# Optimization experiments

Hardware: AMD Instinct MI355X
Metric: run time of the kernel (lower is better)

Reference implementation:

```python
import jax, jax.numpy as jnp
import numpy as np

N, D, C = 8192, 256, 100
MARGIN = 1.0


def setup_inputs() -> dict:
    key = jax.random.key(0)
    k1, k2 = jax.random.split(key)
    features = jax.random.normal(k1, (N, D), dtype=jnp.float32)
    labels = jax.random.randint(k2, (N,), 0, C, dtype=jnp.int64)
    return {"features": features, "labels": labels}


def _pairwise_dist(f):
    # f: [N, D] L2-normalized rows. Euclidean distance matrix [N, N].
    sq = jnp.sum(f * f, axis=1)  # [N]
    d2 = sq[:, None] + sq[None, :] - 2.0 * (f @ f.T)
    d2 = jnp.maximum(d2, 0.0)
    # safe sqrt: zero distance (incl. diagonal) -> 0 with finite grad
    pos = d2 > 0.0
    return jnp.where(pos, jnp.sqrt(jnp.where(pos, d2, 1.0)), 0.0)


def reference(features, labels):
    # F.normalize(p=2, dim=1)
    norm = jnp.linalg.norm(features, axis=1, keepdims=True)
    f = features / jnp.maximum(norm, 1e-12)

    dist = _pairwise_dist(f)  # [N, N]

    onehot = jax.nn.one_hot(labels, C, dtype=f.dtype)  # [N, C]
    counts = jnp.sum(onehot, axis=0)  # [C]
    # S[a, b] = sum_{i in a, j in b} dist[i, j]
    S = onehot.T @ dist @ onehot  # [C, C]

    # intra: per-class mean over off-diagonal pairs (diag of dist is 0),
    # only classes with count > 1, then mean over those classes
    intra_valid = counts > 1.0
    intra_denom = jnp.where(intra_valid, counts * (counts - 1.0), 1.0)
    intra_per_class = jnp.diag(S) / intra_denom
    n_intra = jnp.sum(intra_valid.astype(f.dtype))
    intra = jnp.where(
        n_intra > 0,
        jnp.sum(jnp.where(intra_valid, intra_per_class, 0.0)) / jnp.maximum(n_intra, 1.0),
        0.0,
    )

    # inter: per class-pair (a < b, both present) mean distance, then mean over pairs
    pair_cnt = counts[:, None] * counts[None, :]
    inter_mat = S / jnp.where(pair_cnt > 0.0, pair_cnt, 1.0)
    present = counts > 0.0
    upper = jnp.triu(jnp.ones((C, C), dtype=bool), k=1)
    pair_mask = upper & present[:, None] & present[None, :]
    n_pairs = jnp.sum(pair_mask.astype(f.dtype))
    inter = jnp.where(
        n_pairs > 0,
        jnp.sum(jnp.where(pair_mask, inter_mat, 0.0)) / jnp.maximum(n_pairs, 1.0),
        1.0,
    )

    loss = jax.nn.relu(intra - inter + MARGIN)
    return loss  # scalar; .mean() of a scalar is itself
```

## Files before the change

### kernel.cpp

```cpp
#include <hip/hip_runtime.h>
#include <math.h>

#define N_ROWS 8192
#define D_DIM  256
#define C_CLS  100
#define BM 128
#define BK 128
#define NSTRIP (N_ROWS / BM)
#define NBLK (NSTRIP * (NSTRIP + 1) / 2)
#define UPK (C_CLS * (C_CLS + 1) / 2)
#define MAXSEG 4

typedef __attribute__((ext_vector_type(4))) float floatx4;

__device__ __forceinline__ void gl2lds16(const void* g, void* l) {
    __builtin_amdgcn_global_load_lds(
        (const __attribute__((address_space(1))) void*)g,
        (__attribute__((address_space(3))) void*)l, 16, 0, 0);
}

__global__ void sort_k(const int* __restrict__ labels, int* __restrict__ dest,
                       int* __restrict__ slab, int* __restrict__ offs,
                       float* __restrict__ Ug) {
    __shared__ int h[C_CLS];
    __shared__ int oS[C_CLS + 1];
    __shared__ int cur[C_CLS];
    const int t = threadIdx.x;
    if (t < C_CLS) h[t] = 0;
    __syncthreads();
    int myl[8];
#pragma unroll
    for (int u = 0; u < 8; ++u) myl[u] = labels[t + u * 1024];
#pragma unroll
    for (int u = 0; u < 8; ++u) atomicAdd(&h[myl[u]], 1);
    __syncthreads();
    if (t == 0) {
        int run = 0;
        for (int c = 0; c < C_CLS; ++c) { oS[c] = run; run += h[c]; }
        oS[C_CLS] = run;
    }
    __syncthreads();
    if (t < C_CLS) cur[t] = oS[t];
    __syncthreads();
#pragma unroll
    for (int u = 0; u < 8; ++u) {
        const int i = t + u * 1024;
        const int pos = atomicAdd(&cur[myl[u]], 1);
        dest[i] = pos;
        slab[pos] = myl[u];
    }
    if (t < C_CLS + 1) offs[t] = oS[t];
    for (int e = t; e < UPK; e += 1024) Ug[e] = 0.f;
}

__global__ void normalize_k(const float* __restrict__ in, const int* __restrict__ dest,
                            unsigned int* __restrict__ fnb8) {
    const int row  = blockIdx.x * 4 + (threadIdx.x >> 6);
    const int lane = threadIdx.x & 63;
    float4 v = ((const float4*)in)[row * 64 + lane];
    float s = v.x * v.x + v.y * v.y + v.z * v.z + v.w * v.w;
#pragma unroll
    for (int o = 32; o > 0; o >>= 1) s += __shfl_xor(s, o, 64);
    const float inv = 1.f / fmaxf(sqrtf(s), 1e-12f);
    const int d = dest[row];
    int pk = __builtin_amdgcn_cvt_pk_fp8_f32(v.x * inv, v.y * inv, 0, 0);
    pk     = __builtin_amdgcn_cvt_pk_fp8_f32(v.z * inv, v.w * inv, pk, 1);
    fnb8[d * 64 + lane] = (unsigned int)pk;
}

__global__ __launch_bounds__(256, 4)
void main_k(const unsigned char* __restrict__ fnb8, const int* __restrict__ slab,
            const int* __restrict__ offs_g, float* __restrict__ Ug) {
    __shared__ __align__(16) unsigned char As[BM * BK];
    __shared__ __align__(16) unsigned char Bs[BM * BK];
    __shared__ float red[4][MAXSEG * MAXSEG][17];
    __shared__ int soffs[C_CLS + 1];
    __shared__ int meta[4][4];

    const int t = threadIdx.x;

    int b = blockIdx.x, ti = 0, len = NSTRIP;
    while (b >= len) { b -= len; ++ti; --len; }
    const int tj = ti + b;
    const int i0 = ti * BM, j0 = tj * BM;

    if (t < C_CLS + 1) soffs[t] = offs_g[t];

    const int lane = t & 63;
    const int w    = t >> 6;
    const int m0 = (w & 1) * 64, n0 = (w >> 1) * 64;
    const int lr = lane & 15, lq = lane >> 4;
    const int swz = (lr >> 1) & 7;

    int abase[4], bbase[4];
#pragma unroll
    for (int mb = 0; mb < 4; ++mb) abase[mb] = (m0 + mb * 16 + lr) * BK;
#pragma unroll
    for (int nb = 0; nb < 4; ++nb) bbase[nb] = (n0 + nb * 16 + lr) * BK;

    int srow[4], skc[4];
#pragma unroll
    for (int u = 0; u < 4; ++u) {
        const int s = t + 256 * u;
        srow[u] = s >> 3;
        skc[u]  = (s & 7) ^ ((srow[u] >> 1) & 7);
    }

    floatx4 acc[4][4];
#pragma unroll
    for (int mb = 0; mb < 4; ++mb)
#pragma unroll
        for (int nb = 0; nb < 4; ++nb) acc[mb][nb] = 0.f;

#pragma unroll
    for (int k0 = 0; k0 < D_DIM; k0 += BK) {
        __syncthreads();
#pragma unroll
        for (int u = 0; u < 4; ++u)
            gl2lds16(&fnb8[(size_t)(i0 + srow[u]) * D_DIM + k0 + skc[u] * 16],
                     &As[(t + 256 * u) * 16]);
#pragma unroll
        for (int u = 0; u < 4; ++u)
            gl2lds16(&fnb8[(size_t)(j0 + srow[u]) * D_DIM + k0 + skc[u] * 16],
                     &Bs[(t + 256 * u) * 16]);
        __syncthreads();

#pragma unroll
        for (int si = 0; si < 4; ++si) {
            const int coff = ((((si * 2) + (lq >> 1)) ^ swz) << 4) + ((lq & 1) << 3);
            long a[4], bb[4];
#pragma unroll
            for (int mb = 0; mb < 4; ++mb) a[mb]  = *(const long*)&As[abase[mb] + coff];
#pragma unroll
            for (int nb = 0; nb < 4; ++nb) bb[nb] = *(const long*)&Bs[bbase[nb] + coff];
#pragma unroll
            for (int mb = 0; mb < 4; ++mb)
#pragma unroll
                for (int nb = 0; nb < 4; ++nb)
                    acc[mb][nb] = __builtin_amdgcn_mfma_f32_16x16x32_fp8_fp8(
                        a[mb], bb[nb], acc[mb][nb], 0, 0, 0);
        }
    }

    const bool diag = (ti == tj);
#pragma unroll
    for (int mb = 0; mb < 4; ++mb)
#pragma unroll
        for (int nb = 0; nb < 4; ++nb)
#pragma unroll
            for (int r = 0; r < 4; ++r) {
                const float g = acc[mb][nb][r];
                float dv = __builtin_amdgcn_sqrtf(fmaxf(2.f - 2.f * g, 0.f));
                const int rt = m0 + mb * 16 + lq * 4 + r;
                const int ct = n0 + nb * 16 + lr;
                if (diag && rt == ct) dv = 0.f;
                acc[mb][nb][r] = dv;
            }

    const int cA0 = __builtin_amdgcn_readfirstlane(slab[i0 + m0]);
    const int cA1 = __builtin_amdgcn_readfirstlane(slab[i0 + m0 + 63]);
    const int cB0 = __builtin_amdgcn_readfirstlane(slab[j0 + n0]);
    const int cB1 = __builtin_amdgcn_readfirstlane(slab[j0 + n0 + 63]);
    const int segsA = cA1 - cA0 + 1, segsB = cB1 - cB0 + 1;
    if (lane == 0) { meta[w][0] = cA0; meta[w][1] = cB0; meta[w][2] = segsA; meta[w][3] = segsB; }
    const float wscale = diag ? 1.f : 2.f;

    float rem[4][4];
#pragma unroll
    for (int mb = 0; mb < 4; ++mb)
#pragma unroll
        for (int r = 0; r < 4; ++r)
            rem[mb][r] = acc[mb][0][r] + acc[mb][1][r] + acc[mb][2][r] + acc[mb][3][r];

    for (int sb = 0; sb < segsB; ++sb) {
        const int cb = cB0 + sb;
        float colsum[4][4];
        if (sb == segsB - 1) {
#pragma unroll
            for (int mb = 0; mb < 4; ++mb)
#pragma unroll
                for (int r = 0; r < 4; ++r) colsum[mb][r] = rem[mb][r];
        } else {
            const int rb0 = max(soffs[cb]     - j0, n0);
            const int rb1 = min(soffs[cb + 1] - j0, n0 + 64);
#pragma unroll
            for (int mb = 0; mb < 4; ++mb)
#pragma unroll
                for (int r = 0; r < 4; ++r) colsum[mb][r] = 0.f;
#pragma unroll
            for (int nb = 0; nb < 4; ++nb) {
                const int ct = n0 + nb * 16 + lr;
                const float mk = ((ct >= rb0) & (ct < rb1)) ? 1.f : 0.f;
#pragma unroll
                for (int mb = 0; mb < 4; ++mb)
#pragma unroll
                    for (int r = 0; r < 4; ++r)
                        colsum[mb][r] = fmaf(mk, acc[mb][nb][r], colsum[mb][r]);
            }
#pragma unroll
            for (int mb = 0; mb < 4; ++mb)
#pragma unroll
                for (int r = 0; r < 4; ++r) rem[mb][r] -= colsum[mb][r];
        }
        for (int sa = 0; sa < segsA; ++sa) {
            const int ca = cA0 + sa;
            const int ra0 = max(soffs[ca]     - i0, m0);
            const int ra1 = min(soffs[ca + 1] - i0, m0 + 64);
            float v = 0.f;
#pragma unroll
            for (int mb = 0; mb < 4; ++mb) {
                const int rtb = m0 + mb * 16 + lq * 4;
#pragma unroll
                for (int r = 0; r < 4; ++r) {
                    const int rt = rtb + r;
                    const bool ir = (rt >= ra0) & (rt < ra1);
                    v += ir ? colsum[mb][r] : 0.f;
                }
            }
            if (sa < MAXSEG && sb < MAXSEG) {
                v += __shfl_xor(v, 1, 64);
                v += __shfl_xor(v, 2, 64);
                if ((lane & 3) == 0) red[w][sb * MAXSEG + sa][lane >> 2] = v;
            } else {
#pragma unroll
                for (int o = 32; o > 0; o >>= 1) v += __shfl_xor(v, o, 64);
                if (lane == 0 && v != 0.f) {
                    const int mn = min(ca, cb), mx = max(ca, cb);
                    atomicAdd(&Ug[mx + ((mn * (2 * C_CLS - 1 - mn)) >> 1)], wscale * v);
                }
            }
        }
    }

    __syncthreads();
    {
        const int combo = t >> 2, q = t & 3;
        const int wv = combo >> 4, sl = combo & 15;
        float s = red[wv][sl][q * 4 + 0] + red[wv][sl][q * 4 + 1]
                + red[wv][sl][q * 4 + 2] + red[wv][sl][q * 4 + 3];
        s += __shfl_xor(s, 1, 64);
        s += __shfl_xor(s, 2, 64);
        const int sa = sl & (MAXSEG - 1), sb = sl >> 2;
        if (q == 0 && sa < meta[wv][2] && sb < meta[wv][3] && s != 0.f) {
            const int ca = meta[wv][0] + sa, cb = meta[wv][1] + sb;
            const int mn = min(ca, cb), mx = max(ca, cb);
            atomicAdd(&Ug[mx + ((mn * (2 * C_CLS - 1 - mn)) >> 1)], wscale * s);
        }
    }
}

__global__ void finalize_k(const float* __restrict__ U, const int* __restrict__ offs,
                           float* __restrict__ out) {
    __shared__ int   cnt[C_CLS];
    __shared__ float rf[256];
    __shared__ int   ri[256];
    const int t = threadIdx.x;
    if (t < C_CLS) cnt[t] = offs[t + 1] - offs[t];
    __syncthreads();

    float s_intra = 0.f; int n_intra = 0;
    if (t < C_CLS) {
        int c = cnt[t];
        if (c > 1) {
            int idx = t + ((t * (2 * C_CLS - 1 - t)) >> 1);
            s_intra = U[idx] / ((float)c * (float)(c - 1));
            n_intra = 1;
        }
    }
    float s_inter = 0.f; int n_pairs = 0;
    for (int p = t; p < C_CLS * C_CLS; p += 256) {
        int a = p / C_CLS, b2 = p - a * C_CLS;
        if (b2 > a && cnt[a] > 0 && cnt[b2] > 0) {
            int idx = b2 + ((a * (2 * C_CLS - 1 - a)) >> 1);
            s_inter += 0.5f * U[idx] / ((float)cnt[a] * (float)cnt[b2]);
            ++n_pairs;
        }
    }

    rf[t] = s_intra; ri[t] = n_intra; __syncthreads();
    for (int s = 128; s > 0; s >>= 1) {
        if (t < s) { rf[t] += rf[t + s]; ri[t] += ri[t + s]; }
        __syncthreads();
    }
    float intra_sum = rf[0]; int intra_n = ri[0];
    __syncthreads();
    rf[t] = s_inter; ri[t] = n_pairs; __syncthreads();
    for (int s = 128; s > 0; s >>= 1) {
        if (t < s) { rf[t] += rf[t + s]; ri[t] += ri[t + s]; }
        __syncthreads();
    }
    if (t == 0) {
        float inter_sum = rf[0]; int pairs_n = ri[0];
        float intra = (intra_n > 0) ? intra_sum / (float)intra_n : 0.f;
        float inter = (pairs_n > 0) ? inter_sum / (float)pairs_n : 1.f;
        out[0] = fmaxf(intra - inter + 1.0f, 0.f);
    }
}

extern "C" void kernel_launch(void* const* d_in, const int* in_sizes, int n_in,
                              void* d_out, int out_size, void* d_ws, size_t ws_size,
                              hipStream_t stream) {
    const float* feats  = (const float*)d_in[0];
    const int*   labels = (const int*)d_in[1];
    float* out = (float*)d_out;

    char* p = (char*)d_ws;
    unsigned char* fnb8 = (unsigned char*)p;  p += (size_t)N_ROWS * D_DIM;
    int*   slab = (int*)p;  p += (size_t)N_ROWS * sizeof(int);
    int*   dest = (int*)p;  p += (size_t)N_ROWS * sizeof(int);
    int*   offs = (int*)p;  p += 128 * sizeof(int);
    float* Ug   = (float*)p;

    sort_k     <<<1, 1024, 0, stream>>>(labels, dest, slab, offs, Ug);
    normalize_k<<<N_ROWS / 4, 256, 0, stream>>>(feats, dest, (unsigned int*)fnb8);
    main_k     <<<NBLK, 256, 0, stream>>>(fnb8, slab, offs, Ug);
    finalize_k <<<1, 256, 0, stream>>>(Ug, offs, out);
}
```

Baseline: 109.2 us.

## Load full K tile once, fuse finalize via last-block counter, parallel scan

The GEMM loop now loads the whole 256-wide K extent of both tiles into one 64KB shared buffer and runs a single sync instead of two K-steps. Scratch reduction arrays are aliased into that buffer, and launch bounds drop to 2 blocks per CU. The separate finalize kernel is folded into main_k through an atomic ticket counter, so the last block computes the loss and one launch is saved. The serial prefix sum in sort_k becomes a wavefront shuffle scan. The trade-off is lower occupancy and less overlap between loads and MFMA.

```diff
diff --git a/kernel.cpp b/kernel.cpp
--- a/kernel.cpp
+++ b/kernel.cpp
@@ -5,7 +5,6 @@
 #define D_DIM  256
 #define C_CLS  100
 #define BM 128
-#define BK 128
 #define NSTRIP (N_ROWS / BM)
 #define NBLK (NSTRIP * (NSTRIP + 1) / 2)
 #define UPK (C_CLS * (C_CLS + 1) / 2)
@@ -21,8 +20,9 @@
 
 __global__ void sort_k(const int* __restrict__ labels, int* __restrict__ dest,
                        int* __restrict__ slab, int* __restrict__ offs,
-                       float* __restrict__ Ug) {
+                       float* __restrict__ Ug, int* __restrict__ ctr) {
     __shared__ int h[C_CLS];
+    __shared__ int incl[128];
     __shared__ int oS[C_CLS + 1];
     __shared__ int cur[C_CLS];
     const int t = threadIdx.x;
@@ -34,11 +34,19 @@
 #pragma unroll
     for (int u = 0; u < 8; ++u) atomicAdd(&h[myl[u]], 1);
     __syncthreads();
-    if (t == 0) {
-        int run = 0;
-        for (int c = 0; c < C_CLS; ++c) { oS[c] = run; run += h[c]; }
-        oS[C_CLS] = run;
-    }
+    if (t < 128) {
+        const int lane = t & 63;
+        int v = (t < C_CLS) ? h[t] : 0;
+#pragma unroll
+        for (int o = 1; o < 64; o <<= 1) {
+            const int n = __shfl_up(v, o, 64);
+            if (lane >= o) v += n;
+        }
+        incl[t] = v;
+    }
+    __syncthreads();
+    if (t <= C_CLS)
+        oS[t] = (t == 0) ? 0 : incl[t - 1] + ((t - 1) >= 64 ? incl[63] : 0);
     __syncthreads();
     if (t < C_CLS) cur[t] = oS[t];
     __syncthreads();
@@ -51,6 +59,7 @@
     }
     if (t < C_CLS + 1) offs[t] = oS[t];
     for (int e = t; e < UPK; e += 1024) Ug[e] = 0.f;
+    if (t == 0) *ctr = 0;
 }
 
 __global__ void normalize_k(const float* __restrict__ in, const int* __restrict__ dest,
@@ -68,14 +77,19 @@
     fnb8[d * 64 + lane] = (unsigned int)pk;
 }
 
-__global__ __launch_bounds__(256, 4)
+__global__ __launch_bounds__(256, 2)
 void main_k(const unsigned char* __restrict__ fnb8, const int* __restrict__ slab,
-            const int* __restrict__ offs_g, float* __restrict__ Ug) {
-    __shared__ __align__(16) unsigned char As[BM * BK];
-    __shared__ __align__(16) unsigned char Bs[BM * BK];
-    __shared__ float red[4][MAXSEG * MAXSEG][17];
-    __shared__ int soffs[C_CLS + 1];
-    __shared__ int meta[4][4];
+            const int* __restrict__ offs_g, float* __restrict__ Ug,
+            int* __restrict__ ctr, float* __restrict__ out) {
+    __shared__ __align__(16) unsigned char smem[65536];
+    unsigned char* const As = smem;
+    unsigned char* const Bs = smem + 32768;
+    float* const red   = (float*)smem;
+    int*   const meta  = (int*)(smem + 4352);
+    int*   const flag  = (int*)(smem + 4416);
+    float* const rf    = (float*)(smem + 4432);
+    int*   const ri    = (int*)(smem + 5456);
+    int*   const soffs = (int*)(smem + 6480);
 
     const int t = threadIdx.x;
 
@@ -83,8 +97,6 @@
     while (b >= len) { b -= len; ++ti; --len; }
     const int tj = ti + b;
     const int i0 = ti * BM, j0 = tj * BM;
-
-    if (t < C_CLS + 1) soffs[t] = offs_g[t];
 
     const int lane = t & 63;
     const int w    = t >> 6;
@@ -94,16 +106,23 @@
 
     int abase[4], bbase[4];
 #pragma unroll
-    for (int mb = 0; mb < 4; ++mb) abase[mb] = (m0 + mb * 16 + lr) * BK;
-#pragma unroll
-    for (int nb = 0; nb < 4; ++nb) bbase[nb] = (n0 + nb * 16 + lr) * BK;
-
-    int srow[4], skc[4];
-#pragma unroll
-    for (int u = 0; u < 4; ++u) {
+    for (int mb = 0; mb < 4; ++mb) abase[mb] = (m0 + mb * 16 + lr) * D_DIM;
+#pragma unroll
+    for (int nb = 0; nb < 4; ++nb) bbase[nb] = (n0 + nb * 16 + lr) * D_DIM;
+
+#pragma unroll
+    for (int u = 0; u < 8; ++u) {
         const int s = t + 256 * u;
-        srow[u] = s >> 3;
-        skc[u]  = (s & 7) ^ ((srow[u] >> 1) & 7);
+        const int row = s >> 4;
+        const int kc  = (s & 15) ^ ((row >> 1) & 7);
+        gl2lds16(&fnb8[(size_t)(i0 + row) * D_DIM + kc * 16], &As[s * 16]);
+    }
+#pragma unroll
+    for (int u = 0; u < 8; ++u) {
+        const int s = t + 256 * u;
+        const int row = s >> 4;
+        const int kc  = (s & 15) ^ ((row >> 1) & 7);
+        gl2lds16(&fnb8[(size_t)(j0 + row) * D_DIM + kc * 16], &Bs[s * 16]);
     }
 
     floatx4 acc[4][4];
@@ -112,35 +131,27 @@
 #pragma unroll
         for (int nb = 0; nb < 4; ++nb) acc[mb][nb] = 0.f;
 
-#pragma unroll
-    for (int k0 = 0; k0 < D_DIM; k0 += BK) {
-        __syncthreads();
-#pragma unroll
-        for (int u = 0; u < 4; ++u)
-            gl2lds16(&fnb8[(size_t)(i0 + srow[u]) * D_DIM + k0 + skc[u] * 16],
-                     &As[(t + 256 * u) * 16]);
-#pragma unroll
-        for (int u = 0; u < 4; ++u)
-            gl2lds16(&fnb8[(size_t)(j0 + srow[u]) * D_DIM + k0 + skc[u] * 16],
-                     &Bs[(t + 256 * u) * 16]);
-        __syncthreads();
-
-#pragma unroll
-        for (int si = 0; si < 4; ++si) {
-            const int coff = ((((si * 2) + (lq >> 1)) ^ swz) << 4) + ((lq & 1) << 3);
-            long a[4], bb[4];
-#pragma unroll
-            for (int mb = 0; mb < 4; ++mb) a[mb]  = *(const long*)&As[abase[mb] + coff];
-#pragma unroll
-            for (int nb = 0; nb < 4; ++nb) bb[nb] = *(const long*)&Bs[bbase[nb] + coff];
-#pragma unroll
-            for (int mb = 0; mb < 4; ++mb)
-#pragma unroll
-                for (int nb = 0; nb < 4; ++nb)
-                    acc[mb][nb] = __builtin_amdgcn_mfma_f32_16x16x32_fp8_fp8(
-                        a[mb], bb[nb], acc[mb][nb], 0, 0, 0);
-        }
-    }
+    __syncthreads();
+
+#pragma unroll
+    for (int si = 0; si < 8; ++si) {
+        const int coff = ((((si * 2) + (lq >> 1)) ^ swz) << 4) + ((lq & 1) << 3);
+        long a[4], bb[4];
+#pragma unroll
+        for (int mb = 0; mb < 4; ++mb) a[mb]  = *(const long*)&As[abase[mb] + coff];
+#pragma unroll
+        for (int nb = 0; nb < 4; ++nb) bb[nb] = *(const long*)&Bs[bbase[nb] + coff];
+#pragma unroll
+        for (int mb = 0; mb < 4; ++mb)
+#pragma unroll
+            for (int nb = 0; nb < 4; ++nb)
+                acc[mb][nb] = __builtin_amdgcn_mfma_f32_16x16x32_fp8_fp8(
+                    a[mb], bb[nb], acc[mb][nb], 0, 0, 0);
+    }
+
+    __syncthreads();
+
+    if (t < C_CLS + 1) soffs[t] = offs_g[t];
 
     const bool diag = (ti == tj);
 #pragma unroll
@@ -162,7 +173,10 @@
     const int cB0 = __builtin_amdgcn_readfirstlane(slab[j0 + n0]);
     const int cB1 = __builtin_amdgcn_readfirstlane(slab[j0 + n0 + 63]);
     const int segsA = cA1 - cA0 + 1, segsB = cB1 - cB0 + 1;
-    if (lane == 0) { meta[w][0] = cA0; meta[w][1] = cB0; meta[w][2] = segsA; meta[w][3] = segsB; }
+    if (lane == 0) {
+        meta[w * 4 + 0] = cA0; meta[w * 4 + 1] = cB0;
+        meta[w * 4 + 2] = segsA; meta[w * 4 + 3] = segsB;
+    }
     const float wscale = diag ? 1.f : 2.f;
 
     float rem[4][4];
@@ -171,6 +185,8 @@
 #pragma unroll
         for (int r = 0; r < 4; ++r)
             rem[mb][r] = acc[mb][0][r] + acc[mb][1][r] + acc[mb][2][r] + acc[mb][3][r];
+
+    __syncthreads();
 
     for (int sb = 0; sb < segsB; ++sb) {
         const int cb = cB0 + sb;
@@ -220,7 +236,8 @@
             if (sa < MAXSEG && sb < MAXSEG) {
                 v += __shfl_xor(v, 1, 64);
                 v += __shfl_xor(v, 2, 64);
-                if ((lane & 3) == 0) red[w][sb * MAXSEG + sa][lane >> 2] = v;
+                if ((lane & 3) == 0)
+                    red[(w * 16 + sb * MAXSEG + sa) * 17 + (lane >> 2)] = v;
             } else {
 #pragma unroll
                 for (int o = 32; o > 0; o >>= 1) v += __shfl_xor(v, o, 64);
@@ -236,64 +253,66 @@
     {
         const int combo = t >> 2, q = t & 3;
         const int wv = combo >> 4, sl = combo & 15;
-        float s = red[wv][sl][q * 4 + 0] + red[wv][sl][q * 4 + 1]
-                + red[wv][sl][q * 4 + 2] + red[wv][sl][q * 4 + 3];
+        const float* rp = &red[(wv * 16 + sl) * 17];
+        float s = rp[q * 4 + 0] + rp[q * 4 + 1] + rp[q * 4 + 2] + rp[q * 4 + 3];
         s += __shfl_xor(s, 1, 64);
         s += __shfl_xor(s, 2, 64);
         const int sa = sl & (MAXSEG - 1), sb = sl >> 2;
-        if (q == 0 && sa < meta[wv][2] && sb < meta[wv][3] && s != 0.f) {
-            const int ca = meta[wv][0] + sa, cb = meta[wv][1] + sb;
+        if (q == 0 && sa < meta[wv * 4 + 2] && sb < meta[wv * 4 + 3] && s != 0.f) {
+            const int ca = meta[wv * 4 + 0] + sa, cb = meta[wv * 4 + 1] + sb;
             const int mn = min(ca, cb), mx = max(ca, cb);
             atomicAdd(&Ug[mx + ((mn * (2 * C_CLS - 1 - mn)) >> 1)], wscale * s);
         }
     }
-}
-
-__global__ void finalize_k(const float* __restrict__ U, const int* __restrict__ offs,
-                           float* __restrict__ out) {
-    __shared__ int   cnt[C_CLS];
-    __shared__ float rf[256];
-    __shared__ int   ri[256];
-    const int t = threadIdx.x;
-    if (t < C_CLS) cnt[t] = offs[t + 1] - offs[t];
-    __syncthreads();
-
-    float s_intra = 0.f; int n_intra = 0;
-    if (t < C_CLS) {
-        int c = cnt[t];
-        if (c > 1) {
-            int idx = t + ((t * (2 * C_CLS - 1 - t)) >> 1);
-            s_intra = U[idx] / ((float)c * (float)(c - 1));
-            n_intra = 1;
-        }
-    }
-    float s_inter = 0.f; int n_pairs = 0;
-    for (int p = t; p < C_CLS * C_CLS; p += 256) {
-        int a = p / C_CLS, b2 = p - a * C_CLS;
-        if (b2 > a && cnt[a] > 0 && cnt[b2] > 0) {
-            int idx = b2 + ((a * (2 * C_CLS - 1 - a)) >> 1);
-            s_inter += 0.5f * U[idx] / ((float)cnt[a] * (float)cnt[b2]);
-            ++n_pairs;
-        }
-    }
-
-    rf[t] = s_intra; ri[t] = n_intra; __syncthreads();
-    for (int s = 128; s > 0; s >>= 1) {
-        if (t < s) { rf[t] += rf[t + s]; ri[t] += ri[t + s]; }
+
+    __syncthreads();
+    if (t == 0) {
+        asm volatile("s_waitcnt vmcnt(0)" ::: "memory");
+        *flag = (atomicAdd(ctr, 1) == NBLK - 1) ? 1 : 0;
+    }
+    __syncthreads();
+    if (*flag) {
+        __threadfence();
+        float s_intra = 0.f; int n_intra = 0;
+        if (t < C_CLS) {
+            const int c = soffs[t + 1] - soffs[t];
+            if (c > 1) {
+                const int idx = t + ((t * (2 * C_CLS - 1 - t)) >> 1);
+                s_intra = Ug[idx] / ((float)c * (float)(c - 1));
+                n_intra = 1;
+            }
+        }
+        float s_inter = 0.f; int n_pairs = 0;
+        for (int p = t; p < C_CLS * C_CLS; p += 256) {
+            const int a = p / C_CLS, b2 = p - a * C_CLS;
+            if (b2 > a) {
+                const int ca = soffs[a + 1] - soffs[a];
+                const int cb = soffs[b2 + 1] - soffs[b2];
+                if (ca > 0 && cb > 0) {
+                    const int idx = b2 + ((a * (2 * C_CLS - 1 - a)) >> 1);
+                    s_inter += 0.5f * Ug[idx] / ((float)ca * (float)cb);
+                    ++n_pairs;
+                }
+            }
+        }
+        rf[t] = s_intra; ri[t] = n_intra; __syncthreads();
+        for (int s2 = 128; s2 > 0; s2 >>= 1) {
+            if (t < s2) { rf[t] += rf[t + s2]; ri[t] += ri[t + s2]; }
+            __syncthreads();
+        }
+        const float intra_sum = rf[0]; const int intra_n = ri[0];
         __syncthreads();
-    }
-    float intra_sum = rf[0]; int intra_n = ri[0];
-    __syncthreads();
-    rf[t] = s_inter; ri[t] = n_pairs; __syncthreads();
-    for (int s = 128; s > 0; s >>= 1) {
-        if (t < s) { rf[t] += rf[t + s]; ri[t] += ri[t + s]; }
-        __syncthreads();
-    }
-    if (t == 0) {
-        float inter_sum = rf[0]; int pairs_n = ri[0];
-        float intra = (intra_n > 0) ? intra_sum / (float)intra_n : 0.f;
-        float inter = (pairs_n > 0) ? inter_sum / (float)pairs_n : 1.f;
-        out[0] = fmaxf(intra - inter + 1.0f, 0.f);
+        rf[t] = s_inter; ri[t] = n_pairs; __syncthreads();
+        for (int s2 = 128; s2 > 0; s2 >>= 1) {
+            if (t < s2) { rf[t] += rf[t + s2]; ri[t] += ri[t + s2]; }
+            __syncthreads();
+        }
+        if (t == 0) {
+            const float inter_sum = rf[0]; const int pairs_n = ri[0];
+            const float intra = (intra_n > 0) ? intra_sum / (float)intra_n : 0.f;
+            const float inter = (pairs_n > 0) ? inter_sum / (float)pairs_n : 1.f;
+            out[0] = fmaxf(intra - inter + 1.0f, 0.f);
+        }
     }
 }
 
@@ -309,10 +328,10 @@
     int*   slab = (int*)p;  p += (size_t)N_ROWS * sizeof(int);
     int*   dest = (int*)p;  p += (size_t)N_ROWS * sizeof(int);
     int*   offs = (int*)p;  p += 128 * sizeof(int);
-    float* Ug   = (float*)p;
-
-    sort_k     <<<1, 1024, 0, stream>>>(labels, dest, slab, offs, Ug);
+    float* Ug   = (float*)p;  p += ((UPK + 31) / 32) * 32 * sizeof(float);
+    int*   ctr  = (int*)p;
+
+    sort_k     <<<1, 1024, 0, stream>>>(labels, dest, slab, offs, Ug, ctr);
     normalize_k<<<N_ROWS / 4, 256, 0, stream>>>(feats, dest, (unsigned int*)fnb8);
-    main_k     <<<NBLK, 256, 0, stream>>>(fnb8, slab, offs, Ug);
-    finalize_k <<<1, 256, 0, stream>>>(Ug, offs, out);
-}
+    main_k     <<<NBLK, 256, 0, stream>>>(fnb8, slab, offs, Ug, ctr, out);
+}
```

Measured after the change: 124.4 us. 1.14x slower.
